# Optimization experiments

Hardware: AMD Instinct MI355X
Metric: run time of the kernel (lower is better)

Reference implementation:

```python
import jax, jax.numpy as jnp
import numpy as np

CHUNK = 64
H = 8
EPS = 1e-5

def _rmsnorm(x, w):
    var = jnp.mean(x * x, axis=-1, keepdims=True)
    return x * jax.lax.rsqrt(var + EPS) * w

def setup_inputs() -> dict:
    key = jax.random.key(0)
    ks = jax.random.split(key, 16)
    B, T, D = 2, 8192, 1024
    Dh = D // H  # 128
    s = 0.02
    inp = {
        "hidden_states": jax.random.normal(ks[0], (B, T, D), jnp.float32),
        "output_attentions": 0,
        "q_w": jax.random.normal(ks[1], (D, D), jnp.float32) * s,
        "k_w": jax.random.normal(ks[2], (D, D), jnp.float32) * s,
        "v_w": jax.random.normal(ks[3], (D, D), jnp.float32) * s,
        "o_w": jax.random.normal(ks[4], (D, D), jnp.float32) * s,
        "fmq_w1": jax.random.normal(ks[5], (Dh, Dh), jnp.float32) * s,
        "fmq_b1": jnp.zeros((Dh,), jnp.float32),
        "fmq_w2": jax.random.normal(ks[6], (Dh, Dh), jnp.float32) * s,
        "fmq_b2": jnp.zeros((Dh,), jnp.float32),
        "fmk_w1": jax.random.normal(ks[7], (Dh, Dh), jnp.float32) * s,
        "fmk_b1": jnp.zeros((Dh,), jnp.float32),
        "fmk_w2": jax.random.normal(ks[8], (Dh, Dh), jnp.float32) * s,
        "fmk_b2": jnp.zeros((Dh,), jnp.float32),
        "rms_w": jnp.ones((Dh,), jnp.float32),
    }
    return inp

def reference(hidden_states, output_attentions, q_w, k_w, v_w, o_w,
              fmq_w1, fmq_b1, fmq_w2, fmq_b2,
              fmk_w1, fmk_b1, fmk_w2, fmk_b2, rms_w):
    B, T, D = hidden_states.shape
    Dk = D // H
    Dv = D // H
    # projections (no bias)
    q = (hidden_states @ q_w.T).reshape(B, T, H, Dk)
    k = (hidden_states @ k_w.T).reshape(B, T, H, Dk)
    v = (hidden_states @ v_w.T).reshape(B, T, H, Dv)
    # Hadamard feature map: layer1(x) * layer2(x), per-head Linear with bias
    phi_q = (q @ fmq_w1.T + fmq_b1) * (q @ fmq_w2.T + fmq_b2)
    phi_k = (k @ fmk_w1.T + fmk_b1) * (k @ fmk_w2.T + fmk_b2)
    # chunked causal linear attention, scale = Dk**-0.5 (fla default)
    scale = Dk ** -0.5
    N = T // CHUNK
    qc = (phi_q * scale).reshape(B, N, CHUNK, H, Dk)
    kc = phi_k.reshape(B, N, CHUNK, H, Dk)
    vc = v.reshape(B, N, CHUNK, H, Dv)
    # per-chunk kv outer products and exclusive prefix state
    kv = jnp.einsum('bnchk,bnchv->bnhkv', kc, vc)
    S = jnp.cumsum(kv, axis=1)
    S_excl = jnp.concatenate([jnp.zeros_like(S[:, :1]), S[:, :-1]], axis=1)
    # intra-chunk causal attention
    A = jnp.einsum('bnchk,bnshk->bnhcs', qc, kc)
    mask = jnp.tril(jnp.ones((CHUNK, CHUNK), dtype=bool))
    A = jnp.where(mask, A, 0.0)
    o = jnp.einsum('bnhcs,bnshv->bnchv', A, vc)
    o = o + jnp.einsum('bnchk,bnhkv->bnchv', qc, S_excl)
    o = o.reshape(B, T, H, Dv)
    o = _rmsnorm(o, rms_w)
    o = o.reshape(B, T, H * Dv) @ o_w.T
    return o
```

## Files before the change

### kernel.cpp

```cpp
#include <hip/hip_runtime.h>
#include <hip/hip_bf16.h>
#include <stdint.h>

#define B_     2
#define T_     8192
#define D_     1024
#define H_     8
#define DH     128
#define RTOT   (B_*T_)
#define NSC    16
#define NCHUNK 8

typedef __attribute__((ext_vector_type(8))) short bf16x8;
typedef __attribute__((ext_vector_type(4))) float f32x4;

__device__ __forceinline__ void gload16(void* lds, const void* g) {
  __builtin_amdgcn_global_load_lds(
      (const __attribute__((address_space(1))) unsigned int*)g,
      (__attribute__((address_space(3))) unsigned int*)lds, 16, 0, 0);
}

__device__ __forceinline__ short bf16bits(float v) {
  __hip_bfloat16 h = __float2bfloat16(v);
  return *reinterpret_cast<short*>(&h);
}
__device__ __forceinline__ float bf16val(short s) {
  __hip_bfloat16 h = *reinterpret_cast<__hip_bfloat16*>(&s);
  return __bfloat162float(h);
}

__global__ void split_hl(const float* __restrict__ x, __hip_bfloat16* __restrict__ hi,
                         __hip_bfloat16* __restrict__ lo, int n) {
  int stride = gridDim.x * blockDim.x;
  for (int i = blockIdx.x * blockDim.x + threadIdx.x; i < n; i += stride) {
    float v = x[i];
    __hip_bfloat16 h = __float2bfloat16(v);
    hi[i] = h;
    lo[i] = __float2bfloat16(v - __bfloat162float(h));
  }
}

__global__ void split_cat(const float* __restrict__ w1, const float* __restrict__ w2,
                          __hip_bfloat16* __restrict__ hi, __hip_bfloat16* __restrict__ lo) {
  int i = blockIdx.x * 256 + threadIdx.x;
  float v = (i < 16384) ? w1[i] : w2[i - 16384];
  __hip_bfloat16 h = __float2bfloat16(v);
  hi[i] = h;
  lo[i] = __float2bfloat16(v - __bfloat162float(h));
}

__global__ __launch_bounds__(256, 2) void gemm_f32a(
    const float* __restrict__ A, const __hip_bfloat16* __restrict__ Bh,
    const __hip_bfloat16* __restrict__ Bl, float* __restrict__ C, int M, int N, int K)
{
  __shared__ __align__(16) float          sAf[128*64];
  __shared__ __align__(16) __hip_bfloat16 sBh[128*64];
  __shared__ __align__(16) __hip_bfloat16 sBl[128*64];

  const int tid  = threadIdx.x;
  const int lane = tid & 63;
  const int wave = tid >> 6;
  const int wr = (wave >> 1) * 64;
  const int wc = (wave & 1) * 64;
  const int row0 = blockIdx.x * 128;
  const int col0 = blockIdx.y * 128;

  f32x4 acc[4][4];
  #pragma unroll
  for (int i = 0; i < 4; ++i)
    #pragma unroll
    for (int j = 0; j < 4; ++j) acc[i][j] = (f32x4){0.f, 0.f, 0.f, 0.f};

  for (int k0 = 0; k0 < K; k0 += 64) {
    #pragma unroll
    for (int seg = 0; seg < 8; ++seg) {
      const int p = tid * 16 + seg * 4096;
      const int r = p >> 8;
      const int q = (p & 255) ^ ((r & 7) << 4);
      gload16((char*)sAf + p, (const char*)A + ((size_t)(row0 + r) * K + k0) * 4 + q);
    }
    #pragma unroll
    for (int seg = 0; seg < 4; ++seg) {
      const int p = tid * 16 + seg * 4096;
      const int r = p >> 7;
      const int q = (p & 127) ^ ((r & 7) << 4);
      const size_t gb = (size_t)(col0 + r) * K * 2 + (size_t)(2 * k0 + q);
      gload16((char*)sBh + p, (const char*)Bh + gb);
      gload16((char*)sBl + p, (const char*)Bl + gb);
    }
    __syncthreads();

    #pragma unroll
    for (int kk = 0; kk < 2; ++kk) {
      bf16x8 ah[4], al[4], bh[4], bl[4];
      #pragma unroll
      for (int mi = 0; mi < 4; ++mi) {
        const int r = wr + mi * 16 + (lane & 15);
        const int g0p = kk * 8 + ((lane >> 4) << 1);
        const int g0 = g0p ^ (r & 7), g1 = (g0p + 1) ^ (r & 7);
        const f32x4 x0 = *(const f32x4*)&sAf[r * 64 + (g0 << 2)];
        const f32x4 x1 = *(const f32x4*)&sAf[r * 64 + (g1 << 2)];
        #pragma unroll
        for (int e = 0; e < 4; ++e) {
          const float v0 = x0[e], v1 = x1[e];
          const short h0 = bf16bits(v0), h1 = bf16bits(v1);
          ah[mi][e] = h0;     ah[mi][e + 4] = h1;
          al[mi][e] = bf16bits(v0 - bf16val(h0));
          al[mi][e + 4] = bf16bits(v1 - bf16val(h1));
        }
      }
      #pragma unroll
      for (int ni = 0; ni < 4; ++ni) {
        const int r = wc + ni * 16 + (lane & 15);
        const int off = ((r << 7) + kk * 64 + ((lane >> 4) << 4)) ^ ((r & 7) << 4);
        bh[ni] = *(const bf16x8*)((const char*)sBh + off);
        bl[ni] = *(const bf16x8*)((const char*)sBl + off);
      }
      #pragma unroll
      for (int mi = 0; mi < 4; ++mi)
        #pragma unroll
        for (int ni = 0; ni < 4; ++ni) {
          acc[mi][ni] = __builtin_amdgcn_mfma_f32_16x16x32_bf16(al[mi], bh[ni], acc[mi][ni], 0, 0, 0);
          acc[mi][ni] = __builtin_amdgcn_mfma_f32_16x16x32_bf16(ah[mi], bl[ni], acc[mi][ni], 0, 0, 0);
          acc[mi][ni] = __builtin_amdgcn_mfma_f32_16x16x32_bf16(ah[mi], bh[ni], acc[mi][ni], 0, 0, 0);
        }
    }
    __syncthreads();
  }

  #pragma unroll
  for (int mi = 0; mi < 4; ++mi) {
    const int rb = row0 + wr + mi * 16 + ((lane >> 4) << 2);
    #pragma unroll
    for (int ni = 0; ni < 4; ++ni) {
      const int c = col0 + wc + ni * 16 + (lane & 15);
      #pragma unroll
      for (int rg = 0; rg < 4; ++rg)
        C[(size_t)(rb + rg) * N + c] = acc[mi][ni][rg];
    }
  }
}

__global__ __launch_bounds__(512, 1) void featuremap2(
    float* XP, const __hip_bfloat16* __restrict__ Wh, const __hip_bfloat16* __restrict__ Wl,
    const float* __restrict__ B1v, const float* __restrict__ B2v)
{
  __shared__ __align__(16) char smem[98304];
  float*          sAf = (float*)smem;
  __hip_bfloat16* sBh = (__hip_bfloat16*)(smem + 32768);
  __hip_bfloat16* sBl = (__hip_bfloat16*)(smem + 65536);

  const int tid  = threadIdx.x;
  const int lane = tid & 63;
  const int wave = tid >> 6;
  const int wr = (wave >> 2) * 64;
  const int wc = (wave & 3) * 64;
  const int row0 = blockIdx.x * 128;
  const int h    = blockIdx.y;

  f32x4 acc[4][4];
  #pragma unroll
  for (int i = 0; i < 4; ++i)
    #pragma unroll
    for (int j = 0; j < 4; ++j) acc[i][j] = (f32x4){0.f, 0.f, 0.f, 0.f};

  for (int k0 = 0; k0 < 128; k0 += 64) {
    #pragma unroll
    for (int seg = 0; seg < 4; ++seg) {
      const int p = tid * 16 + seg * 8192;
      const int r = p >> 8;
      const int q = (p & 255) ^ ((r & 7) << 4);
      gload16((char*)sAf + p,
              (const char*)XP + ((size_t)(row0 + r) * D_ + h * DH + k0) * 4 + q);
    }
    #pragma unroll
    for (int seg = 0; seg < 4; ++seg) {
      const int p = tid * 16 + seg * 8192;
      const int r = p >> 7;
      const int q = (p & 127) ^ ((r & 7) << 4);
      const size_t gb = (size_t)r * 256 + (size_t)(2 * k0 + q);
      gload16((char*)sBh + p, (const char*)Wh + gb);
      gload16((char*)sBl + p, (const char*)Wl + gb);
    }
    __syncthreads();

    #pragma unroll
    for (int kk = 0; kk < 2; ++kk) {
      bf16x8 ah[4], al[4], bh[4], bl[4];
      #pragma unroll
      for (int mi = 0; mi < 4; ++mi) {
        const int r = wr + mi * 16 + (lane & 15);
        const int g0p = kk * 8 + ((lane >> 4) << 1);
        const int g0 = g0p ^ (r & 7), g1 = (g0p + 1) ^ (r & 7);
        const f32x4 x0 = *(const f32x4*)&sAf[r * 64 + (g0 << 2)];
        const f32x4 x1 = *(const f32x4*)&sAf[r * 64 + (g1 << 2)];
        #pragma unroll
        for (int e = 0; e < 4; ++e) {
          const float v0 = x0[e], v1 = x1[e];
          const short h0 = bf16bits(v0), h1 = bf16bits(v1);
          ah[mi][e] = h0;     ah[mi][e + 4] = h1;
          al[mi][e] = bf16bits(v0 - bf16val(h0));
          al[mi][e + 4] = bf16bits(v1 - bf16val(h1));
        }
      }
      #pragma unroll
      for (int ni = 0; ni < 4; ++ni) {
        const int r = wc + ni * 16 + (lane & 15);
        const int off = ((r << 7) + kk * 64 + ((lane >> 4) << 4)) ^ ((r & 7) << 4);
        bh[ni] = *(const bf16x8*)((const char*)sBh + off);
        bl[ni] = *(const bf16x8*)((const char*)sBl + off);
      }
      #pragma unroll
      for (int mi = 0; mi < 4; ++mi)
        #pragma unroll
        for (int ni = 0; ni < 4; ++ni) {
          acc[mi][ni] = __builtin_amdgcn_mfma_f32_16x16x32_bf16(al[mi], bh[ni], acc[mi][ni], 0, 0, 0);
          acc[mi][ni] = __builtin_amdgcn_mfma_f32_16x16x32_bf16(ah[mi], bl[ni], acc[mi][ni], 0, 0, 0);
          acc[mi][ni] = __builtin_amdgcn_mfma_f32_16x16x32_bf16(ah[mi], bh[ni], acc[mi][ni], 0, 0, 0);
        }
    }
    __syncthreads();
  }

  float* sEp = (float*)smem;
  if (wc < 128) {
    #pragma unroll
    for (int mi = 0; mi < 4; ++mi) {
      const int rb = wr + mi * 16 + ((lane >> 4) << 2);
      #pragma unroll
      for (int ni = 0; ni < 4; ++ni) {
        const int col = wc + ni * 16 + (lane & 15);
        const float b1 = B1v[col];
        #pragma unroll
        for (int rg = 0; rg < 4; ++rg)
          sEp[(rb + rg) * 132 + col] = acc[mi][ni][rg] + b1;
      }
    }
  }
  __syncthreads();
  if (wc >= 128) {
    #pragma unroll
    for (int mi = 0; mi < 4; ++mi) {
      const int rb = wr + mi * 16 + ((lane >> 4) << 2);
      #pragma unroll
      for (int ni = 0; ni < 4; ++ni) {
        const int c2 = wc - 128 + ni * 16 + (lane & 15);
        const float b2 = B2v[c2];
        #pragma unroll
        for (int rg = 0; rg < 4; ++rg) {
          const int row = rb + rg;
          XP[(size_t)(row0 + row) * D_ + h * DH + c2] =
              sEp[row * 132 + c2] * (acc[mi][ni][rg] + b2);
        }
      }
    }
  }
}

__global__ __launch_bounds__(256, 2) void skv_kernel(
    const float* __restrict__ PK, const float* __restrict__ V, float* __restrict__ SKV)
{
  __shared__ __align__(16) float sk[64 * 128];
  __shared__ __align__(16) float sv[64 * 128];
  const int tid = threadIdx.x;
  const int tx = tid & 15, ty = tid >> 4;
  const int sc = blockIdx.x, h = blockIdx.y, b = blockIdx.z;
  const size_t R0 = (size_t)b * T_ + sc * 512;

  f32x4 acc[8][2];
  #pragma unroll
  for (int i = 0; i < 8; ++i)
    #pragma unroll
    for (int g = 0; g < 2; ++g) acc[i][g] = (f32x4){0.f, 0.f, 0.f, 0.f};

  for (int sub = 0; sub < 8; ++sub) {
    __syncthreads();
    for (int i4 = tid; i4 < 2048; i4 += 256) {
      const int idx = i4 * 4;
      const int r = idx >> 7, col = idx & 127;
      const size_t gofs = (R0 + sub * 64 + r) * D_ + h * DH + col;
      *(f32x4*)&sk[idx] = *(const f32x4*)&PK[gofs];
      *(f32x4*)&sv[idx] = *(const f32x4*)&V[gofs];
    }
    __syncthreads();
    for (int c = 0; c < 64; ++c) {
      float kv[8];
      #pragma unroll
      for (int i = 0; i < 8; ++i) kv[i] = sk[c * 128 + ty + 16 * i];
      const f32x4 v0 = *(const f32x4*)&sv[c * 128 + tx * 4];
      const f32x4 v1 = *(const f32x4*)&sv[c * 128 + 64 + tx * 4];
      #pragma unroll
      for (int i = 0; i < 8; ++i)
        #pragma unroll
        for (int j = 0; j < 4; ++j) {
          acc[i][0][j] = fmaf(kv[i], v0[j], acc[i][0][j]);
          acc[i][1][j] = fmaf(kv[i], v1[j], acc[i][1][j]);
        }
    }
  }
  float* outp = SKV + ((size_t)(b * H_ + h) * NSC + sc) * 16384;
  #pragma unroll
  for (int i = 0; i < 8; ++i)
    #pragma unroll
    for (int g = 0; g < 2; ++g)
      *(f32x4*)&outp[(ty + 16 * i) * 128 + g * 64 + tx * 4] = acc[i][g];
}

__global__ void skv_prefix(float* __restrict__ SKV) {
  const int e = blockIdx.x * 256 + threadIdx.x;
  float* p = SKV + (size_t)(blockIdx.z * H_ + blockIdx.y) * NSC * 16384 + e;
  float s = 0.f;
  #pragma unroll
  for (int sc = 0; sc < NSC; ++sc) {
    const float x = p[(size_t)sc * 16384];
    p[(size_t)sc * 16384] = s;
    s += x;
  }
}

__global__ __launch_bounds__(512, 1) void fused_attn(
    const float* PQ, const float* PK, const float* V,
    const float* __restrict__ SKVp, const float* __restrict__ rmsw, float* O)
{
  __shared__ __align__(16) float sS [128 * 128];
  __shared__ __align__(16) float sQt[128 * 64];
  __shared__ __align__(16) float sKt[128 * 64];
  __shared__ __align__(16) float sV [64 * 128];

  const int tid  = threadIdx.x;
  const int lane = tid & 63;
  const int tx = tid & 15, ty = tid >> 4;
  const int sc = blockIdx.x, h = blockIdx.y, b = blockIdx.z;
  const size_t R0 = (size_t)b * T_ + sc * 512;
  const float qscale = 0.08838834764831843f;

  f32x4 rw[2];
  #pragma unroll
  for (int g = 0; g < 2; ++g) rw[g] = *(const f32x4*)&rmsw[g * 64 + tx * 4];

  {
    const float* slab = SKVp + ((size_t)(b * H_ + h) * NSC + sc) * 16384;
    for (int i = tid; i < 4096; i += 512)
      *(f32x4*)&sS[i * 4] = *(const f32x4*)&slab[i * 4];
  }
  __syncthreads();

  const int cst = tid & 63;
  const int kq  = tid >> 6;

  for (int m = 0; m < NCHUNK; ++m) {
    const size_t rbase = R0 + m * 64;

    {
      const float* qp = PQ + (rbase + cst) * D_ + h * DH + kq * 16;
      const float* kp = PK + (rbase + cst) * D_ + h * DH + kq * 16;
      #pragma unroll
      for (int t = 0; t < 4; ++t) {
        const f32x4 qv = *(const f32x4*)(qp + t * 4);
        const f32x4 kv = *(const f32x4*)(kp + t * 4);
        #pragma unroll
        for (int e = 0; e < 4; ++e) {
          const int k = kq * 16 + t * 4 + e;
          sQt[k * 64 + cst] = qv[e] * qscale;
          sKt[k * 64 + cst] = kv[e];
        }
      }
    }
    for (int i = tid; i < 2048; i += 512) {
      const int idx = i * 4;
      const int c2 = idx >> 7, v0 = idx & 127;
      *(f32x4*)&sV[idx] = *(const f32x4*)&V[(rbase + c2) * D_ + h * DH + v0];
    }
    __syncthreads();

    float a[2][4] = {};
    for (int k = 0; k < 128; ++k) {
      const float2 q2 = *(const float2*)&sQt[k * 64 + ty * 2];
      const f32x4  k4 = *(const f32x4*)&sKt[k * 64 + tx * 4];
      #pragma unroll
      for (int j = 0; j < 4; ++j) {
        a[0][j] = fmaf(q2.x, k4[j], a[0][j]);
        a[1][j] = fmaf(q2.y, k4[j], a[1][j]);
      }
    }
    #pragma unroll
    for (int i = 0; i < 2; ++i)
      #pragma unroll
      for (int j = 0; j < 4; ++j)
        if (tx * 4 + j > ty * 2 + i) a[i][j] = 0.f;

    float o[2][2][4] = {};

    for (int tq = 0; tq < 16; ++tq) {
      const int src = (lane & 48) | tq;
      f32x4 vv[4][2];
      #pragma unroll
      for (int j = 0; j < 4; ++j)
        #pragma unroll
        for (int g = 0; g < 2; ++g)
          vv[j][g] = *(const f32x4*)&sV[(tq * 4 + j) * 128 + g * 64 + tx * 4];
      #pragma unroll
      for (int i = 0; i < 2; ++i) {
        float av[4];
        #pragma unroll
        for (int j = 0; j < 4; ++j) av[j] = __shfl(a[i][j], src);
        #pragma unroll
        for (int j = 0; j < 4; ++j)
          #pragma unroll
          for (int g = 0; g < 2; ++g)
            #pragma unroll
            for (int jj = 0; jj < 4; ++jj)
              o[i][g][jj] = fmaf(av[j], vv[j][g][jj], o[i][g][jj]);
      }
    }

    for (int k = 0; k < 128; ++k) {
      const float2 q2 = *(const float2*)&sQt[k * 64 + ty * 2];
      #pragma unroll
      for (int g = 0; g < 2; ++g) {
        const f32x4 sv = *(const f32x4*)&sS[k * 128 + g * 64 + tx * 4];
        #pragma unroll
        for (int j = 0; j < 4; ++j) {
          o[0][g][j] = fmaf(q2.x, sv[j], o[0][g][j]);
          o[1][g][j] = fmaf(q2.y, sv[j], o[1][g][j]);
        }
      }
    }
    __syncthreads();

    {
      f32x4 Sacc[4][2];
      #pragma unroll
      for (int i = 0; i < 4; ++i)
        #pragma unroll
        for (int g = 0; g < 2; ++g)
          Sacc[i][g] = *(const f32x4*)&sS[(ty + 32 * i) * 128 + g * 64 + tx * 4];
      for (int c = 0; c < 64; ++c) {
        f32x4 vvg[2];
        #pragma unroll
        for (int g = 0; g < 2; ++g)
          vvg[g] = *(const f32x4*)&sV[c * 128 + g * 64 + tx * 4];
        float kc[4];
        #pragma unroll
        for (int i = 0; i < 4; ++i) kc[i] = sKt[(ty + 32 * i) * 64 + c];
        #pragma unroll
        for (int i = 0; i < 4; ++i)
          #pragma unroll
          for (int g = 0; g < 2; ++g)
            #pragma unroll
            for (int j = 0; j < 4; ++j)
              Sacc[i][g][j] = fmaf(kc[i], vvg[g][j], Sacc[i][g][j]);
      }
      #pragma unroll
      for (int i = 0; i < 4; ++i)
        #pragma unroll
        for (int g = 0; g < 2; ++g)
          *(f32x4*)&sS[(ty + 32 * i) * 128 + g * 64 + tx * 4] = Sacc[i][g];
    }

    #pragma unroll
    for (int i = 0; i < 2; ++i) {
      float ss = 0.f;
      #pragma unroll
      for (int g = 0; g < 2; ++g)
        #pragma unroll
        for (int j = 0; j < 4; ++j) ss += o[i][g][j] * o[i][g][j];
      ss += __shfl_xor(ss, 1); ss += __shfl_xor(ss, 2);
      ss += __shfl_xor(ss, 4); ss += __shfl_xor(ss, 8);
      const float inv = 1.f / sqrtf(ss * (1.f / 128.f) + 1e-5f);
      #pragma unroll
      for (int g = 0; g < 2; ++g) {
        f32x4 ov;
        #pragma unroll
        for (int j = 0; j < 4; ++j) ov[j] = o[i][g][j] * inv * rw[g][j];
        *(f32x4*)&O[(rbase + ty * 2 + i) * D_ + h * DH + g * 64 + tx * 4] = ov;
      }
    }
    __syncthreads();
  }
}

extern "C" void kernel_launch(void* const* d_in, const int* in_sizes, int n_in,
                              void* d_out, int out_size, void* d_ws, size_t ws_size,
                              hipStream_t stream) {
  const float* hs = (const float*)d_in[0];
  const float* wsrc[4] = {(const float*)d_in[2], (const float*)d_in[3],
                          (const float*)d_in[4], (const float*)d_in[5]};
  const float* fmq_w1 = (const float*)d_in[6];
  const float* fmq_b1 = (const float*)d_in[7];
  const float* fmq_w2 = (const float*)d_in[8];
  const float* fmq_b2 = (const float*)d_in[9];
  const float* fmk_w1 = (const float*)d_in[10];
  const float* fmk_b1 = (const float*)d_in[11];
  const float* fmk_w2 = (const float*)d_in[12];
  const float* fmk_b2 = (const float*)d_in[13];
  const float* rmsw   = (const float*)d_in[14];
  float* out = (float*)d_out;

  char* ws = (char*)d_ws;
  const size_t MB = 1ull << 20;
  float* q = (float*)ws;
  float* k = (float*)(ws + 64 * MB);
  __hip_bfloat16* w_h[4]; __hip_bfloat16* w_l[4];
  for (int i = 0; i < 4; ++i) {
    w_h[i] = (__hip_bfloat16*)(ws + 128 * MB + (size_t)i * 4 * MB);
    w_l[i] = (__hip_bfloat16*)(ws + 128 * MB + (size_t)i * 4 * MB + 2 * MB);
  }
  float* SKV = (float*)(ws + 144 * MB);
  __hip_bfloat16* wcq_h = (__hip_bfloat16*)(ws + 144 * MB);
  __hip_bfloat16* wcq_l = (__hip_bfloat16*)(ws + 144 * MB + 64 * 1024);
  __hip_bfloat16* wck_h = (__hip_bfloat16*)(ws + 144 * MB + 128 * 1024);
  __hip_bfloat16* wck_l = (__hip_bfloat16*)(ws + 144 * MB + 192 * 1024);
  float* v = (float*)d_out;

  for (int i = 0; i < 4; ++i)
    split_hl<<<512, 256, 0, stream>>>(wsrc[i], w_h[i], w_l[i], D_ * D_);
  split_cat<<<128, 256, 0, stream>>>(fmq_w1, fmq_w2, wcq_h, wcq_l);
  split_cat<<<128, 256, 0, stream>>>(fmk_w1, fmk_w2, wck_h, wck_l);

  dim3 gg(RTOT / 128, D_ / 128);
  gemm_f32a<<<gg, 256, 0, stream>>>(hs, w_h[0], w_l[0], q, RTOT, D_, D_);
  gemm_f32a<<<gg, 256, 0, stream>>>(hs, w_h[1], w_l[1], k, RTOT, D_, D_);
  gemm_f32a<<<gg, 256, 0, stream>>>(hs, w_h[2], w_l[2], v, RTOT, D_, D_);

  featuremap2<<<dim3(RTOT / 128, H_), 512, 0, stream>>>(q, wcq_h, wcq_l, fmq_b1, fmq_b2);
  featuremap2<<<dim3(RTOT / 128, H_), 512, 0, stream>>>(k, wck_h, wck_l, fmk_b1, fmk_b2);

  skv_kernel<<<dim3(NSC, H_, B_), 256, 0, stream>>>(k, v, SKV);
  skv_prefix<<<dim3(64, H_, B_), 256, 0, stream>>>(SKV);

  fused_attn<<<dim3(NSC, H_, B_), 512, 0, stream>>>(q, k, v, SKV, rmsw, q);

  gemm_f32a<<<gg, 256, 0, stream>>>(q, w_h[3], w_l[3], out, RTOT, D_, D_);
}
```

Before: 955.6 us.

## Retile f32 GEMM waves to 32x128 strips and use truncation-based bf16 split

After: 906.6 us. -5.1%, faster.

```diff
diff --git a/kernel.cpp b/kernel.cpp
--- a/kernel.cpp
+++ b/kernel.cpp
@@ -29,6 +29,21 @@
   return __bfloat162float(h);
 }
 
+__device__ __forceinline__ void split8(const f32x4 x0, const f32x4 x1,
+                                       bf16x8& hi, bf16x8& lo) {
+  #pragma unroll
+  for (int e = 0; e < 4; ++e) {
+    const unsigned u0 = __builtin_bit_cast(unsigned, x0[e]);
+    const float hf0 = __builtin_bit_cast(float, u0 & 0xFFFF0000u);
+    hi[e] = (short)(u0 >> 16);
+    lo[e] = (short)(__builtin_bit_cast(unsigned, x0[e] - hf0) >> 16);
+    const unsigned u1 = __builtin_bit_cast(unsigned, x1[e]);
+    const float hf1 = __builtin_bit_cast(float, u1 & 0xFFFF0000u);
+    hi[e + 4] = (short)(u1 >> 16);
+    lo[e + 4] = (short)(__builtin_bit_cast(unsigned, x1[e] - hf1) >> 16);
+  }
+}
+
 __global__ void split_hl(const float* __restrict__ x, __hip_bfloat16* __restrict__ hi,
                          __hip_bfloat16* __restrict__ lo, int n) {
   int stride = gridDim.x * blockDim.x;
@@ -60,16 +75,15 @@
   const int tid  = threadIdx.x;
   const int lane = tid & 63;
   const int wave = tid >> 6;
-  const int wr = (wave >> 1) * 64;
-  const int wc = (wave & 1) * 64;
+  const int wr = wave * 32;
   const int row0 = blockIdx.x * 128;
   const int col0 = blockIdx.y * 128;
 
-  f32x4 acc[4][4];
-  #pragma unroll
-  for (int i = 0; i < 4; ++i)
-    #pragma unroll
-    for (int j = 0; j < 4; ++j) acc[i][j] = (f32x4){0.f, 0.f, 0.f, 0.f};
+  f32x4 acc[2][8];
+  #pragma unroll
+  for (int i = 0; i < 2; ++i)
+    #pragma unroll
+    for (int j = 0; j < 8; ++j) acc[i][j] = (f32x4){0.f, 0.f, 0.f, 0.f};
 
   for (int k0 = 0; k0 < K; k0 += 64) {
     #pragma unroll
@@ -92,48 +106,39 @@
 
     #pragma unroll
     for (int kk = 0; kk < 2; ++kk) {
-      bf16x8 ah[4], al[4], bh[4], bl[4];
-      #pragma unroll
-      for (int mi = 0; mi < 4; ++mi) {
+      bf16x8 ah[2], al[2];
+      #pragma unroll
+      for (int mi = 0; mi < 2; ++mi) {
         const int r = wr + mi * 16 + (lane & 15);
         const int g0p = kk * 8 + ((lane >> 4) << 1);
         const int g0 = g0p ^ (r & 7), g1 = (g0p + 1) ^ (r & 7);
         const f32x4 x0 = *(const f32x4*)&sAf[r * 64 + (g0 << 2)];
         const f32x4 x1 = *(const f32x4*)&sAf[r * 64 + (g1 << 2)];
-        #pragma unroll
-        for (int e = 0; e < 4; ++e) {
-          const float v0 = x0[e], v1 = x1[e];
-          const short h0 = bf16bits(v0), h1 = bf16bits(v1);
-          ah[mi][e] = h0;     ah[mi][e + 4] = h1;
-          al[mi][e] = bf16bits(v0 - bf16val(h0));
-          al[mi][e + 4] = bf16bits(v1 - bf16val(h1));
-        }
-      }
-      #pragma unroll
-      for (int ni = 0; ni < 4; ++ni) {
-        const int r = wc + ni * 16 + (lane & 15);
+        split8(x0, x1, ah[mi], al[mi]);
+      }
+      #pragma unroll
+      for (int ni = 0; ni < 8; ++ni) {
+        const int r = ni * 16 + (lane & 15);
         const int off = ((r << 7) + kk * 64 + ((lane >> 4) << 4)) ^ ((r & 7) << 4);
-        bh[ni] = *(const bf16x8*)((const char*)sBh + off);
-        bl[ni] = *(const bf16x8*)((const char*)sBl + off);
-      }
-      #pragma unroll
-      for (int mi = 0; mi < 4; ++mi)
-        #pragma unroll
-        for (int ni = 0; ni < 4; ++ni) {
-          acc[mi][ni] = __builtin_amdgcn_mfma_f32_16x16x32_bf16(al[mi], bh[ni], acc[mi][ni], 0, 0, 0);
-          acc[mi][ni] = __builtin_amdgcn_mfma_f32_16x16x32_bf16(ah[mi], bl[ni], acc[mi][ni], 0, 0, 0);
-          acc[mi][ni] = __builtin_amdgcn_mfma_f32_16x16x32_bf16(ah[mi], bh[ni], acc[mi][ni], 0, 0, 0);
-        }
-    }
-    __syncthreads();
-  }
-
-  #pragma unroll
-  for (int mi = 0; mi < 4; ++mi) {
+        const bf16x8 bh = *(const bf16x8*)((const char*)sBh + off);
+        const bf16x8 bl = *(const bf16x8*)((const char*)sBl + off);
+        #pragma unroll
+        for (int mi = 0; mi < 2; ++mi) {
+          acc[mi][ni] = __builtin_amdgcn_mfma_f32_16x16x32_bf16(al[mi], bh, acc[mi][ni], 0, 0, 0);
+          acc[mi][ni] = __builtin_amdgcn_mfma_f32_16x16x32_bf16(ah[mi], bl, acc[mi][ni], 0, 0, 0);
+          acc[mi][ni] = __builtin_amdgcn_mfma_f32_16x16x32_bf16(ah[mi], bh, acc[mi][ni], 0, 0, 0);
+        }
+      }
+    }
+    __syncthreads();
+  }
+
+  #pragma unroll
+  for (int mi = 0; mi < 2; ++mi) {
     const int rb = row0 + wr + mi * 16 + ((lane >> 4) << 2);
     #pragma unroll
-    for (int ni = 0; ni < 4; ++ni) {
-      const int c = col0 + wc + ni * 16 + (lane & 15);
+    for (int ni = 0; ni < 8; ++ni) {
+      const int c = col0 + ni * 16 + (lane & 15);
       #pragma unroll
       for (int rg = 0; rg < 4; ++rg)
         C[(size_t)(rb + rg) * N + c] = acc[mi][ni][rg];
```
